# Performance work log

Measured on AMD Instinct MI355X. Metric: run time of the kernel, lower is better.

## Reference

```python
import jax, jax.numpy as jnp
import numpy as np

B = 2048
TT_IN = (16, 16, 16)    # prod = 4096
TT_OUT = (16, 16, 16)   # prod = 4096
BOND = (32, 32)
INIT_STD = 0.05  # keras 'random_normal' default stddev


def setup_inputs() -> dict:
    key = jax.random.key(0)
    k_x, k1, k2, k3 = jax.random.split(key, 4)
    x = jax.random.normal(k_x, (B, int(np.prod(TT_IN))), dtype=jnp.float32)
    core1 = jax.random.normal(k1, (TT_IN[0], TT_OUT[0], BOND[0]), dtype=jnp.float32) * INIT_STD
    core2 = jax.random.normal(k2, (TT_IN[1], TT_OUT[1], BOND[0], BOND[1]), dtype=jnp.float32) * INIT_STD
    core3 = jax.random.normal(k3, (TT_IN[2], TT_OUT[2], BOND[1]), dtype=jnp.float32) * INIT_STD
    bias = jnp.zeros(TT_OUT, dtype=jnp.float32)
    return {"x": x, "core1": core1, "core2": core2, "core3": core3, "bias": bias}


def reference(x, core1, core2, core3, bias):
    # x: [B, 4096] -> [B, x, y, z] tensor-train input modes
    xt = x.reshape((x.shape[0],) + TT_IN)
    # TT contraction: modes x,y,z contracted with cores; a,b,c are output
    # modes; p,q are bond indices (matches original einsum structure for
    # 3 cores: x[1,2,3], c1[1,4,7], c2[2,5,7,8], c3[3,6,8] -> [4,5,6]).
    out = jnp.einsum('nxyz,xap,ybpq,zcq->nabc', xt, core1, core2, core3,
                     optimize='optimal')
    out = out + bias  # bias broadcast over batch, shape TT_OUT
    out = out.reshape(x.shape[0], -1)  # [B, prod(TT_OUT)]
    return jax.nn.relu(out)
```

## Files before the change

### kernel.cpp

```cpp
#include <hip/hip_runtime.h>
#include <hip/hip_bf16.h>
#include <stdint.h>


typedef short bf16x8 __attribute__((ext_vector_type(8)));
typedef float f32x4  __attribute__((ext_vector_type(4)));

#define MB 2048
#define KD 4096
#define ND 4096

__device__ __forceinline__ unsigned short f32_bf16(float f) {
  union { float f; uint32_t u; } v; v.f = f;
  return (unsigned short)((v.u + 0x7fffu + ((v.u >> 16) & 1u)) >> 16);
}
__device__ __forceinline__ float bf2f(unsigned short u) {
  union { uint32_t i; float f; } v; v.i = ((uint32_t)u) << 16; return v.f;
}

__global__ __launch_bounds__(256) void k_prep(const float* __restrict__ x,
                                              const float* __restrict__ c1,
                                              const float* __restrict__ c2,
                                              const float* __restrict__ c3,
                                              unsigned short* __restrict__ xb,
                                              unsigned short* __restrict__ Wt) {
  __shared__ unsigned short sh[17472];
  int bid = blockIdx.x;
  int t = threadIdx.x;

  if (bid < 4096) {
    int i = bid * 256 + t;
    const float4* x4 = (const float4*)x;
    float4 a = x4[2*i];
    float4 b = x4[2*i+1];
    ushort4 lo, hi;
    lo.x = f32_bf16(a.x); lo.y = f32_bf16(a.y); lo.z = f32_bf16(a.z); lo.w = f32_bf16(a.w);
    hi.x = f32_bf16(b.x); hi.y = f32_bf16(b.y); hi.z = f32_bf16(b.z); hi.w = f32_bf16(b.w);
    ushort4* o = (ushort4*)xb;
    o[2*i]   = lo;
    o[2*i+1] = hi;
    return;
  }

  int ab = bid - 4096;
  int a = ab >> 4, b = ab & 15;
  unsigned short* c2s = sh;
  float* c1s = (float*)(sh + 16448);

  #pragma unroll
  for (int y = 0; y < 16; ++y) {
    float4 v = *(const float4*)(c2 + (size_t)(y*16 + b)*1024 + t*4);
    ushort4 s;
    s.x = f32_bf16(v.x); s.y = f32_bf16(v.y); s.z = f32_bf16(v.z); s.w = f32_bf16(v.w);
    *(ushort4*)(c2s + y*1028 + t*4) = s;
  }
  c1s[t]       = c1[((t>>5)*16 + a)*32 + (t&31)];
  c1s[t+256]   = c1[(((t>>5)+8)*16 + a)*32 + (t&31)];
  __syncthreads();

  int xx = t >> 4, yy = t & 15;
  const float* c1r = c1s + xx*32;
  const unsigned short* c2r = c2s + yy*1028;
  float acc[32];
  #pragma unroll
  for (int q = 0; q < 32; ++q) acc[q] = 0.f;
  #pragma unroll 8
  for (int p = 0; p < 32; ++p) {
    float w = c1r[p];
    #pragma unroll
    for (int j = 0; j < 8; ++j) {
      ushort4 v = *(const ushort4*)(c2r + p*32 + j*4);
      acc[4*j+0] = fmaf(w, bf2f(v.x), acc[4*j+0]);
      acc[4*j+1] = fmaf(w, bf2f(v.y), acc[4*j+1]);
      acc[4*j+2] = fmaf(w, bf2f(v.z), acc[4*j+2]);
      acc[4*j+3] = fmaf(w, bf2f(v.w), acc[4*j+3]);
    }
  }
  __syncthreads();

  unsigned short* T2s  = sh;
  unsigned short* c3ps = sh + 8192;

  #pragma unroll
  for (int j = 0; j < 8; ++j) {
    ushort4 s;
    s.x = f32_bf16(acc[4*j+0]); s.y = f32_bf16(acc[4*j+1]);
    s.z = f32_bf16(acc[4*j+2]); s.w = f32_bf16(acc[4*j+3]);
    *(ushort4*)(T2s + t*32 + j*4) = s;
  }
  #pragma unroll
  for (int r = 0; r < 8; ++r) {
    int i4 = t*8 + r;
    float4 v = *(const float4*)(c3 + (size_t)i4*4);
    int e = i4*4;
    int q = e & 31, zc = e >> 5;
    int z = zc >> 4, c = zc & 15;
    ushort4 s;
    s.x = f32_bf16(v.x); s.y = f32_bf16(v.y); s.z = f32_bf16(v.z); s.w = f32_bf16(v.w);
    *(ushort4*)(c3ps + (c*16 + z)*32 + q) = s;
  }
  __syncthreads();

  int wid = t >> 6, lane = t & 63, l15 = lane & 15, lg = lane >> 4;
  bf16x8 bfv[16];
  #pragma unroll
  for (int nt = 0; nt < 16; ++nt)
    bfv[nt] = *(const bf16x8*)(c3ps + (nt*16 + l15)*32 + lg*8);
  #pragma unroll
  for (int mi = 0; mi < 4; ++mi) {
    int mtile = wid*4 + mi;
    bf16x8 af = *(const bf16x8*)(T2s + (mtile*16 + l15)*32 + lg*8);
    #pragma unroll
    for (int nt = 0; nt < 16; ++nt) {
      f32x4 d = {0.f, 0.f, 0.f, 0.f};
      d = __builtin_amdgcn_mfma_f32_16x16x32_bf16(af, bfv[nt], d, 0, 0, 0);
      size_t jrow = (size_t)(ab*16 + nt) * ND;
      #pragma unroll
      for (int i = 0; i < 4; ++i) {
        int xy = mtile*16 + lg*4 + i;
        Wt[jrow + xy*16 + l15] = f32_bf16(d[i]);
      }
    }
  }
}

__device__ __forceinline__ void gload_lds16(const unsigned short* g, unsigned short* l) {
  __builtin_amdgcn_global_load_lds(
      (const __attribute__((address_space(1))) void*)g,
      (__attribute__((address_space(3))) void*)l, 16, 0, 0);
}

__global__ __launch_bounds__(256, 2) void k_gemm(const unsigned short* __restrict__ A,
                                                 const unsigned short* __restrict__ Bw,
                                                 const float* __restrict__ bias,
                                                 float* __restrict__ C) {
  __shared__ unsigned short As[128*64];
  __shared__ unsigned short Bs[128*64];
  int t = threadIdx.x;
  int wid = t >> 6, lane = t & 63;
  int l15 = lane & 15, lg = lane >> 4;
  int m0 = blockIdx.y * 128;
  int n0 = blockIdx.x * 128;
  int wr = wid >> 1, wc = wid & 1;

  int scol = (((t & 7) ^ ((t >> 3) & 7)) * 8);
  int lds_off = t * 8;
  const unsigned short* Ag = A  + (size_t)(m0 + (t >> 3))*KD + scol;
  const unsigned short* Bg = Bw + (size_t)(n0 + (t >> 3))*KD + scol;

  int xr = l15 & 7;

  f32x4 acc[4][4];
  #pragma unroll
  for (int m = 0; m < 4; ++m)
    #pragma unroll
    for (int n = 0; n < 4; ++n)
      acc[m][n] = (f32x4){0.f, 0.f, 0.f, 0.f};

  for (int kt = 0; kt < KD/64; ++kt) {
    int kb = kt * 64;
    #pragma unroll
    for (int s = 0; s < 4; ++s) {
      gload_lds16(Ag + kb + (size_t)s*32*KD, As + lds_off + s*2048);
      gload_lds16(Bg + kb + (size_t)s*32*KD, Bs + lds_off + s*2048);
    }
    __syncthreads();
    bf16x8 aF[2][4], bF[2][4];
    #pragma unroll
    for (int kk = 0; kk < 2; ++kk) {
      int pc = ((kk*4 + lg) ^ xr) * 8;
      #pragma unroll
      for (int m = 0; m < 4; ++m)
        aF[kk][m] = *(const bf16x8*)(As + (wr*64 + m*16 + l15)*64 + pc);
      #pragma unroll
      for (int n = 0; n < 4; ++n)
        bF[kk][n] = *(const bf16x8*)(Bs + (wc*64 + n*16 + l15)*64 + pc);
    }
    #pragma unroll
    for (int kk = 0; kk < 2; ++kk)
      #pragma unroll
      for (int m = 0; m < 4; ++m)
        #pragma unroll
        for (int n = 0; n < 4; ++n)
          acc[m][n] = __builtin_amdgcn_mfma_f32_16x16x32_bf16(aF[kk][m], bF[kk][n],
                                                              acc[m][n], 0, 0, 0);
    __syncthreads();
  }

  #pragma unroll
  for (int m = 0; m < 4; ++m) {
    int gr = m0 + wr*64 + m*16 + lg*4;
    #pragma unroll
    for (int n = 0; n < 4; ++n) {
      int gc = n0 + wc*64 + n*16 + l15;
      float bv = bias[gc];
      #pragma unroll
      for (int i = 0; i < 4; ++i) {
        float v = acc[m][n][i] + bv;
        C[(size_t)(gr + i)*ND + gc] = v > 0.f ? v : 0.f;
      }
    }
  }
}

extern "C" void kernel_launch(void* const* d_in, const int* in_sizes, int n_in,
                              void* d_out, int out_size, void* d_ws, size_t ws_size,
                              hipStream_t stream) {
  (void)in_sizes; (void)n_in; (void)out_size; (void)ws_size;
  const float* x    = (const float*)d_in[0];
  const float* c1   = (const float*)d_in[1];
  const float* c2   = (const float*)d_in[2];
  const float* c3   = (const float*)d_in[3];
  const float* bias = (const float*)d_in[4];
  float* out = (float*)d_out;

  uint8_t* ws = (uint8_t*)d_ws;
  unsigned short* xb = (unsigned short*)(ws);
  unsigned short* Wt = (unsigned short*)(ws + 16777216);

  k_prep<<<4096 + 256, 256, 0, stream>>>(x, c1, c2, c3, xb, Wt);
  k_gemm<<<dim3(ND/128, MB/128), 256, 0, stream>>>(xb, Wt, bias, out);
}
```

Before: 177.8 us.

## Use 256x128 tiles with 8 waves and triple-buffered LDS pipelining

Grows the GEMM block tile to 256x128 with 512 threads and adds a three-stage LDS buffer ring. Global-to-LDS loads for tile k+2 are issued in slices between four MFMA phases, with barriers, waitcnt control and setprio to overlap memory and compute. The aim is to hide load latency that the old load-sync-compute loop exposed. It costs much more LDS, allows only one block per CU, and cuts the grid to 256 blocks, which may underfill the GPU.

Result: slower. 208.5 us (+17.2%).

```diff
diff --git a/kernel.cpp b/kernel.cpp
--- a/kernel.cpp
+++ b/kernel.cpp
@@ -9,6 +9,7 @@
 #define MB 2048
 #define KD 4096
 #define ND 4096
+#define NT_K 64
 
 __device__ __forceinline__ unsigned short f32_bf16(float f) {
   union { float f; uint32_t u; } v; v.f = f;
@@ -130,25 +131,53 @@
       (__attribute__((address_space(3))) void*)l, 16, 0, 0);
 }
 
-__global__ __launch_bounds__(256, 2) void k_gemm(const unsigned short* __restrict__ A,
+template<int H, int KK>
+__device__ __forceinline__ void phase_loads(const unsigned short* Ac, const unsigned short* Bc,
+                                            int wr, int wc, int l15, int lg, int xr,
+                                            bf16x8& a0, bf16x8& a1, bf16x8 (&bF)[2][4]) {
+  const int pc8 = ((KK*4 + lg) ^ xr) * 8;
+  a0 = *(const bf16x8*)(Ac + (wr*64 + (H*2+0)*16 + l15)*64 + pc8);
+  a1 = *(const bf16x8*)(Ac + (wr*64 + (H*2+1)*16 + l15)*64 + pc8);
+  if (H == 0) {
+    #pragma unroll
+    for (int n = 0; n < 4; ++n)
+      bF[KK][n] = *(const bf16x8*)(Bc + (wc*64 + n*16 + l15)*64 + pc8);
+  }
+}
+
+template<int H, int KK>
+__device__ __forceinline__ void phase_fma(const bf16x8& a0, const bf16x8& a1,
+                                          bf16x8 (&bF)[2][4], f32x4 (&acc)[4][4]) {
+  #pragma unroll
+  for (int n = 0; n < 4; ++n) {
+    acc[H*2+0][n] = __builtin_amdgcn_mfma_f32_16x16x32_bf16(a0, bF[KK][n], acc[H*2+0][n], 0, 0, 0);
+    acc[H*2+1][n] = __builtin_amdgcn_mfma_f32_16x16x32_bf16(a1, bF[KK][n], acc[H*2+1][n], 0, 0, 0);
+  }
+}
+
+__global__ __launch_bounds__(512, 1) void k_gemm(const unsigned short* __restrict__ A,
                                                  const unsigned short* __restrict__ Bw,
                                                  const float* __restrict__ bias,
                                                  float* __restrict__ C) {
-  __shared__ unsigned short As[128*64];
-  __shared__ unsigned short Bs[128*64];
-  int t = threadIdx.x;
-  int wid = t >> 6, lane = t & 63;
-  int l15 = lane & 15, lg = lane >> 4;
-  int m0 = blockIdx.y * 128;
-  int n0 = blockIdx.x * 128;
-  int wr = wid >> 1, wc = wid & 1;
-
-  int scol = (((t & 7) ^ ((t >> 3) & 7)) * 8);
-  int lds_off = t * 8;
+  __shared__ unsigned short As[3*256*64];
+  __shared__ unsigned short Bs[3*128*64];
+  const int t = threadIdx.x;
+  const int wid = t >> 6, lane = t & 63;
+  const int l15 = lane & 15, lg = lane >> 4;
+  const int m0 = blockIdx.y * 256;
+  const int n0 = blockIdx.x * 128;
+  const int wr = wid >> 1, wc = wid & 1;
+  const int xr = l15 & 7;
+
+  const int scol = (((t & 7) ^ ((t >> 3) & 7)) * 8);
+  const int t8 = t * 8;
   const unsigned short* Ag = A  + (size_t)(m0 + (t >> 3))*KD + scol;
   const unsigned short* Bg = Bw + (size_t)(n0 + (t >> 3))*KD + scol;
 
-  int xr = l15 & 7;
+#define STG_A(tk, buf, s) gload_lds16(Ag + (size_t)(s)*64*KD + (tk)*64, \
+                                      As + (buf)*16384 + (s)*4096 + t8)
+#define STG_B(tk, buf, s) gload_lds16(Bg + (size_t)(s)*64*KD + (tk)*64, \
+                                      Bs + (buf)*8192  + (s)*4096 + t8)
 
   f32x4 acc[4][4];
   #pragma unroll
@@ -156,35 +185,65 @@
     #pragma unroll
     for (int n = 0; n < 4; ++n)
       acc[m][n] = (f32x4){0.f, 0.f, 0.f, 0.f};
-
-  for (int kt = 0; kt < KD/64; ++kt) {
-    int kb = kt * 64;
-    #pragma unroll
-    for (int s = 0; s < 4; ++s) {
-      gload_lds16(Ag + kb + (size_t)s*32*KD, As + lds_off + s*2048);
-      gload_lds16(Bg + kb + (size_t)s*32*KD, Bs + lds_off + s*2048);
-    }
-    __syncthreads();
-    bf16x8 aF[2][4], bF[2][4];
-    #pragma unroll
-    for (int kk = 0; kk < 2; ++kk) {
-      int pc = ((kk*4 + lg) ^ xr) * 8;
-      #pragma unroll
-      for (int m = 0; m < 4; ++m)
-        aF[kk][m] = *(const bf16x8*)(As + (wr*64 + m*16 + l15)*64 + pc);
-      #pragma unroll
-      for (int n = 0; n < 4; ++n)
-        bF[kk][n] = *(const bf16x8*)(Bs + (wc*64 + n*16 + l15)*64 + pc);
-    }
-    #pragma unroll
-    for (int kk = 0; kk < 2; ++kk)
-      #pragma unroll
-      for (int m = 0; m < 4; ++m)
-        #pragma unroll
-        for (int n = 0; n < 4; ++n)
-          acc[m][n] = __builtin_amdgcn_mfma_f32_16x16x32_bf16(aF[kk][m], bF[kk][n],
-                                                              acc[m][n], 0, 0, 0);
-    __syncthreads();
+  bf16x8 bF[2][4];
+
+  STG_A(0,0,0); STG_A(0,0,1); STG_A(0,0,2); STG_A(0,0,3); STG_B(0,0,0); STG_B(0,0,1);
+  STG_A(1,1,0); STG_A(1,1,1); STG_A(1,1,2); STG_A(1,1,3); STG_B(1,1,0); STG_B(1,1,1);
+  asm volatile("s_waitcnt vmcnt(6)" ::: "memory");
+  __builtin_amdgcn_s_barrier();
+
+  int cur = 0, stg = 2;
+  for (int i = 0; i < NT_K; ++i) {
+    const unsigned short* Ac = As + cur*16384;
+    const unsigned short* Bc = Bs + cur*8192;
+    const int  tk2 = i + 2;
+    const bool do_stage = (i < NT_K - 2);
+    bf16x8 a0, a1;
+
+    phase_loads<0,0>(Ac, Bc, wr, wc, l15, lg, xr, a0, a1, bF);
+    if (do_stage) { STG_A(tk2, stg, 0); STG_A(tk2, stg, 1); }
+    __builtin_amdgcn_s_barrier();
+    asm volatile("s_waitcnt lgkmcnt(0)" ::: "memory");
+    __builtin_amdgcn_sched_barrier(0);
+    __builtin_amdgcn_s_setprio(1);
+    phase_fma<0,0>(a0, a1, bF, acc);
+    __builtin_amdgcn_s_setprio(0);
+    __builtin_amdgcn_s_barrier();
+
+    phase_loads<1,0>(Ac, Bc, wr, wc, l15, lg, xr, a0, a1, bF);
+    if (do_stage) { STG_A(tk2, stg, 2); STG_A(tk2, stg, 3); }
+    __builtin_amdgcn_s_barrier();
+    asm volatile("s_waitcnt lgkmcnt(0)" ::: "memory");
+    __builtin_amdgcn_sched_barrier(0);
+    __builtin_amdgcn_s_setprio(1);
+    phase_fma<1,0>(a0, a1, bF, acc);
+    __builtin_amdgcn_s_setprio(0);
+    __builtin_amdgcn_s_barrier();
+
+    phase_loads<0,1>(Ac, Bc, wr, wc, l15, lg, xr, a0, a1, bF);
+    if (do_stage) { STG_B(tk2, stg, 0); STG_B(tk2, stg, 1); }
+    __builtin_amdgcn_s_barrier();
+    asm volatile("s_waitcnt lgkmcnt(0)" ::: "memory");
+    __builtin_amdgcn_sched_barrier(0);
+    __builtin_amdgcn_s_setprio(1);
+    phase_fma<0,1>(a0, a1, bF, acc);
+    __builtin_amdgcn_s_setprio(0);
+    __builtin_amdgcn_s_barrier();
+
+    phase_loads<1,1>(Ac, Bc, wr, wc, l15, lg, xr, a0, a1, bF);
+    __builtin_amdgcn_s_barrier();
+    asm volatile("s_waitcnt lgkmcnt(0)" ::: "memory");
+    __builtin_amdgcn_sched_barrier(0);
+    __builtin_amdgcn_s_setprio(1);
+    phase_fma<1,1>(a0, a1, bF, acc);
+    __builtin_amdgcn_s_setprio(0);
+
+    if (i < NT_K - 2)       { asm volatile("s_waitcnt vmcnt(6)" ::: "memory"); }
+    else if (i == NT_K - 2) { asm volatile("s_waitcnt vmcnt(0)" ::: "memory"); }
+    __builtin_amdgcn_s_barrier();
+
+    cur = (cur == 2) ? 0 : cur + 1;
+    stg = (stg == 2) ? 0 : stg + 1;
   }
 
   #pragma unroll
@@ -201,6 +260,8 @@
       }
     }
   }
+#undef STG_A
+#undef STG_B
 }
 
 extern "C" void kernel_launch(void* const* d_in, const int* in_sizes, int n_in,
@@ -219,5 +280,5 @@
   unsigned short* Wt = (unsigned short*)(ws + 16777216);
 
   k_prep<<<4096 + 256, 256, 0, stream>>>(x, c1, c2, c3, xb, Wt);
-  k_gemm<<<dim3(ND/128, MB/128), 256, 0, stream>>>(xb, Wt, bias, out);
-}
+  k_gemm<<<dim3(ND/128, MB/256), 512, 0, stream>>>(xb, Wt, bias, out);
+}
```
